# Kernel tuning notes

Measured on AMD Instinct MI355X. Metric: run time of the kernel, lower is better.

The kernel has to match this reference:

```python
import jax, jax.numpy as jnp
import numpy as np

N_NODES = 100000
N_EDGES = 6_400_000
IN_DIM = 128


def gcn_conv(x, W, b, row, col, ew):
    """PyG GCNConv(normalize=True, add_self_loops=True) forward."""
    n = x.shape[0]
    loop = jnp.arange(n)
    row_sl = jnp.concatenate([row, loop])
    col_sl = jnp.concatenate([col, loop])
    ew_sl = jnp.concatenate([ew, jnp.ones((n,), ew.dtype)])
    # symmetric normalization: deg^{-1/2}[src] * w * deg^{-1/2}[dst]
    deg = jax.ops.segment_sum(ew_sl, col_sl, num_segments=n)
    safe_deg = jnp.where(deg > 0, deg, 1.0)
    dis = jnp.where(deg > 0, jax.lax.rsqrt(safe_deg), 0.0)
    norm = dis[row_sl] * ew_sl * dis[col_sl]
    h = x @ W  # [n, out_dim] linear transform first (small out_dim)
    # gather source features, scale, scatter-add into targets
    out = jax.ops.segment_sum(norm[:, None] * h[row_sl], col_sl, num_segments=n)
    return out + b


def setup_inputs() -> dict:
    key = jax.random.key(0)
    ks = jax.random.split(key, 12)
    X = jax.random.normal(ks[0], (N_NODES, IN_DIM), dtype=jnp.float32)
    edge_index = jax.random.randint(ks[1], (2, N_EDGES), 0, N_NODES, dtype=jnp.int64)
    edge_weight = jax.random.uniform(ks[2], (N_EDGES,), dtype=jnp.float32)

    def glorot(k, fan_in, fan_out):
        lim = np.sqrt(6.0 / (fan_in + fan_out)).astype(np.float32)
        return jax.random.uniform(k, (fan_in, fan_out), minval=-lim, maxval=lim, dtype=jnp.float32)

    return {
        "X": X,
        "edge_index": edge_index,
        "edge_weight": edge_weight,
        "W1": glorot(ks[3], IN_DIM, 12), "b1": jnp.zeros((12,), jnp.float32),
        "W2": glorot(ks[4], 12, 6), "b2": jnp.zeros((6,), jnp.float32),
        "W3": glorot(ks[5], 6, 3), "b3": jnp.zeros((3,), jnp.float32),
        "Wl": glorot(ks[6], 3, 1), "bl": jnp.zeros((1,), jnp.float32),
    }


def reference(X, edge_index, edge_weight, W1, b1, W2, b2, W3, b3, Wl, bl):
    row, col = edge_index[0], edge_index[1]
    h = jax.nn.relu(gcn_conv(X, W1, b1, row, col, edge_weight))
    # dropout p=0.2 is identity in eval mode
    h = jax.nn.relu(gcn_conv(h, W2, b2, row, col, edge_weight))
    h = jax.nn.relu(gcn_conv(h, W3, b3, row, col, edge_weight))
    out = jax.nn.sigmoid(h @ Wl + bl)
    return out.squeeze(1)  # [N]
```

## Files before the change

### kernel.cpp

```cpp
#include <hip/hip_runtime.h>
#include <cstdint>
#include <cstddef>

#define RANGE    128
#define RSHIFT   7
#define MAXBUCK  800
#define CSHIFT   12
#define CRANGE   4096
#define MAXC     32
#define FPB      32
#define CH_CNT   8192
#define CH_SC    4096
#define EPT      16
#define PAD      16
#define WSTR     132

typedef _Float16 h8 __attribute__((ext_vector_type(8)));

__global__ void zero_pad_kernel(int* __restrict__ p, int n) {
    int i = blockIdx.x * blockDim.x + threadIdx.x;
    if (i < n) p[i * PAD] = 0;
}

__global__ void count_kernel(const int* __restrict__ col, int* __restrict__ fcnt,
                             int nfine, int E) {
    __shared__ int lcnt[MAXBUCK];
    int tid = threadIdx.x;
    for (int i = tid; i < nfine; i += blockDim.x) lcnt[i] = 0;
    __syncthreads();
    int base = blockIdx.x * CH_CNT;
    int end  = min(E, base + CH_CNT);
    for (int e = base + tid; e < end; e += blockDim.x)
        atomicAdd(&lcnt[col[e] >> RSHIFT], 1);
    __syncthreads();
    for (int i = tid; i < nfine; i += blockDim.x)
        if (lcnt[i]) atomicAdd(&fcnt[i * PAD], lcnt[i]);
}

__global__ void scan_kernel(const int* __restrict__ fcnt, int* __restrict__ fbase,
                            int* __restrict__ fcur, int* __restrict__ cbase,
                            int* __restrict__ ccur, int* __restrict__ row_ptr,
                            int nfine, int ncoarse, int N, int E) {
    __shared__ int lds[1024];
    int T = threadIdx.x;
    int s = (T < nfine) ? fcnt[T * PAD] : 0;
    lds[T] = s;
    __syncthreads();
    for (int off = 1; off < 1024; off <<= 1) {
        int v = (T >= off) ? lds[T - off] : 0;
        __syncthreads();
        lds[T] += v;
        __syncthreads();
    }
    int excl = lds[T] - s;
    if (T < nfine) { fbase[T] = excl; fcur[T * PAD] = excl; }
    if ((T & (FPB - 1)) == 0 && (T >> 5) < ncoarse) {
        cbase[T >> 5] = excl;
        ccur[(T >> 5) * PAD] = excl;
    }
    if (T == 0) { fbase[nfine] = E; cbase[ncoarse] = E; row_ptr[N] = E; }
}

__global__ void coarse_scatter_kernel(const int* __restrict__ row, const int* __restrict__ col,
                                      const float* __restrict__ ew, int* __restrict__ ccur,
                                      uint2* __restrict__ partA, int ncoarse, int E) {
    __shared__ uint2 stage[CH_SC];
    __shared__ unsigned char sb[CH_SC];
    __shared__ int lcnt[MAXC], lofs[MAXC], gofs[MAXC];
    __shared__ int total_s;
    int tid = threadIdx.x;
    if (tid < MAXC) lcnt[tid] = 0;
    __syncthreads();
    int base = blockIdx.x * CH_SC;
    int cnt  = min(E - base, CH_SC);

    uint2 rec[EPT]; int rnk[EPT]; int bb[EPT];
#pragma unroll
    for (int k = 0; k < EPT; k++) {
        int idx = tid + (k << 8);
        if (idx < cnt) {
            int e = base + idx;
            int c = col[e];
            int b = c >> CSHIFT;
            bb[k]  = b;
            rec[k] = make_uint2((unsigned)row[e] | ((unsigned)(c & (CRANGE - 1)) << 17),
                                __float_as_uint(ew[e]));
            rnk[k] = atomicAdd(&lcnt[b], 1);
        }
    }
    __syncthreads();
    if (tid == 0) {
        int run = 0;
        for (int i = 0; i < ncoarse; i++) { lofs[i] = run; run += lcnt[i]; }
        total_s = run;
    }
    __syncthreads();
    if (tid < ncoarse) {
        int c = lcnt[tid];
        if (c) {
            int g = atomicAdd(&ccur[tid * PAD], c);
            gofs[tid] = g - lofs[tid];
        }
    }
#pragma unroll
    for (int k = 0; k < EPT; k++) {
        int idx = tid + (k << 8);
        if (idx < cnt) {
            int p = lofs[bb[k]] + rnk[k];
            stage[p] = rec[k];
            sb[p] = (unsigned char)bb[k];
        }
    }
    __syncthreads();
    int total = total_s;
    for (int i = tid; i < total; i += 256)
        partA[gofs[sb[i]] + i] = stage[i];
}

__global__ void fine_scatter_kernel(const uint2* __restrict__ partA, const int* __restrict__ cbase,
                                    int* __restrict__ fcur, uint2* __restrict__ partB,
                                    int nfine, int ncoarse, int E) {
    __shared__ uint2 stage[CH_SC];
    __shared__ unsigned short sb[CH_SC];
    __shared__ int lcnt[MAXBUCK], lofs[MAXBUCK], gofs[MAXBUCK];
    __shared__ int tmp[256];
    __shared__ int scb[MAXC + 1];
    __shared__ int rlo_s, total_s;
    int tid = threadIdx.x;
    int base = blockIdx.x * CH_SC;
    int cnt  = min(E - base, CH_SC);
    if (tid <= ncoarse) scb[tid] = cbase[tid];
    for (int i = tid; i < nfine; i += 256) lcnt[i] = 0;
    if (tid == 0) {
        int r = 0;
        while (r < ncoarse - 1 && cbase[r + 1] <= base) ++r;
        rlo_s = r;
    }
    __syncthreads();
    int rlo = rlo_s;

    uint2 rec[EPT]; int rnk[EPT]; int ff[EPT];
#pragma unroll
    for (int k = 0; k < EPT; k++) {
        int idx = tid + (k << 8);
        if (idx < cnt) {
            int e = base + idx;
            uint2 v = partA[e];
            int r = rlo;
            while (e >= scb[r + 1]) ++r;
            int col12 = (int)((v.x >> 17) & (CRANGE - 1));
            int f = (r << 5) | (col12 >> RSHIFT);
            ff[k]  = f;
            rec[k] = make_uint2((v.x & 0x1FFFFu) | ((unsigned)(col12 & (RANGE - 1)) << 17), v.y);
            rnk[k] = atomicAdd(&lcnt[f], 1);
        }
    }
    __syncthreads();
    {
        const int Cc = (nfine + 255) >> 8;
        int b0 = tid * Cc;
        int s = 0;
        for (int i = 0; i < Cc; i++) {
            int idx = b0 + i;
            if (idx < nfine) s += lcnt[idx];
        }
        tmp[tid] = s;
        __syncthreads();
        for (int off = 1; off < 256; off <<= 1) {
            int v = (tid >= off) ? tmp[tid - off] : 0;
            __syncthreads();
            tmp[tid] += v;
            __syncthreads();
        }
        int run = tmp[tid] - s;
        for (int i = 0; i < Cc; i++) {
            int idx = b0 + i;
            if (idx < nfine) { lofs[idx] = run; run += lcnt[idx]; }
        }
        if (tid == 255) total_s = tmp[255];
    }
    __syncthreads();
    for (int i = tid; i < nfine; i += 256) {
        int c = lcnt[i];
        if (c) {
            int g = atomicAdd(&fcur[i * PAD], c);
            gofs[i] = g - lofs[i];
        }
    }
#pragma unroll
    for (int k = 0; k < EPT; k++) {
        int idx = tid + (k << 8);
        if (idx < cnt) {
            int p = lofs[ff[k]] + rnk[k];
            stage[p] = rec[k];
            sb[p] = (unsigned short)ff[k];
        }
    }
    __syncthreads();
    int total = total_s;
    for (int i = tid; i < total; i += 256)
        partB[gofs[sb[i]] + i] = stage[i];
}

__global__ void bucket_csr_kernel(const uint2* __restrict__ part, const int* __restrict__ bbase,
                                  int* __restrict__ row_ptr, float* __restrict__ dis,
                                  uint2* __restrict__ csr, int N) {
    __shared__ int   scnt[RANGE];
    __shared__ int   sscan[RANGE];
    __shared__ float sdeg[RANGE];
    __shared__ float sdis[RANGE];
    int b = blockIdx.x, tid = threadIdx.x;
    int s = bbase[b], t = bbase[b + 1];
    if (tid < RANGE) { scnt[tid] = 0; sdeg[tid] = 1.0f; }
    __syncthreads();
    for (int e = s + tid; e < t; e += blockDim.x) {
        uint2 r = part[e];
        int c = (r.x >> 17) & (RANGE - 1);
        atomicAdd(&scnt[c], 1);
        atomicAdd(&sdeg[c], __uint_as_float(r.y));
    }
    __syncthreads();
    int cnt_t = 0;
    if (tid < RANGE) { cnt_t = scnt[tid]; sscan[tid] = cnt_t; }
    __syncthreads();
    for (int off = 1; off < RANGE; off <<= 1) {
        int v = 0;
        if (tid < RANGE && tid >= off) v = sscan[tid - off];
        __syncthreads();
        if (tid < RANGE) sscan[tid] += v;
        __syncthreads();
    }
    if (tid < RANGE) {
        int excl = sscan[tid] - cnt_t;
        int node = b * RANGE + tid;
        float dn = rsqrtf(sdeg[tid]);
        sdis[tid] = dn;
        if (node < N) {
            row_ptr[node] = s + excl;
            dis[node] = dn;
        }
        scnt[tid] = excl;
    }
    __syncthreads();
    for (int e = s + tid; e < t; e += blockDim.x) {
        uint2 r = part[e];
        int c   = (r.x >> 17) & (RANGE - 1);
        int src = (int)(r.x & 0x1FFFFu);
        float v = sdis[c] * __uint_as_float(r.y);
        int off = atomicAdd(&scnt[c], 1);
        csr[s + off] = make_uint2((unsigned)src, __float_as_uint(v));
    }
}

__global__ void lin1_kernel(const float* __restrict__ X, const float* __restrict__ W1,
                            const float* __restrict__ dis, uint4* __restrict__ t1, int n) {
    __shared__ float w1t[12 * WSTR];
    int tid = threadIdx.x;
    for (int i = tid; i < 128 * 12; i += 256) {
        int k = i / 12, o = i - k * 12;
        w1t[o * WSTR + k] = W1[i];
    }
    __syncthreads();
    int gt   = blockIdx.x * 256 + tid;
    int node = gt >> 3;
    int sub  = gt & 7;
    if (node >= n) return;

    const float4* xp = (const float4*)(X + (size_t)node * 128 + sub * 16);
    float4 x0 = xp[0], x1 = xp[1], x2 = xp[2], x3 = xp[3];

    float res[12];
#pragma unroll
    for (int o = 0; o < 12; o++) {
        const float4* wp = (const float4*)(w1t + o * WSTR + sub * 16);
        float4 w0 = wp[0], w1v = wp[1], w2 = wp[2], w3 = wp[3];
        float s;
        s  = x0.x * w0.x + x0.y * w0.y + x0.z * w0.z + x0.w * w0.w;
        s += x1.x * w1v.x + x1.y * w1v.y + x1.z * w1v.z + x1.w * w1v.w;
        s += x2.x * w2.x + x2.y * w2.y + x2.z * w2.z + x2.w * w2.w;
        s += x3.x * w3.x + x3.y * w3.y + x3.z * w3.z + x3.w * w3.w;
        res[o] = s;
    }
#pragma unroll
    for (int o = 0; o < 12; o++) {
        res[o] += __shfl_xor(res[o], 1, 64);
        res[o] += __shfl_xor(res[o], 2, 64);
        res[o] += __shfl_xor(res[o], 4, 64);
    }
    if (sub == 0) {
        h8 a, b;
#pragma unroll
        for (int o = 0; o < 8; o++) a[o] = (_Float16)res[o];
#pragma unroll
        for (int o = 0; o < 4; o++) b[o] = (_Float16)res[8 + o];
#pragma unroll
        for (int o = 4; o < 8; o++) b[o] = (_Float16)0.f;
        uint4 ua = __builtin_bit_cast(uint4, a);
        uint4 ub = __builtin_bit_cast(uint4, b);
        ub.z = __float_as_uint(dis[node]);
        ub.w = 0u;
        uint4* dst = t1 + (size_t)node * 2;
        dst[0] = ua;
        dst[1] = ub;
    }
}

template <int DIN, int ROWW, int DOUT, bool LAST>
__global__ void agg_kernel(const int* __restrict__ row_ptr, const uint2* __restrict__ csr,
                           const uint4* __restrict__ hin,
                           const float* __restrict__ b_this, const float* __restrict__ W_next,
                           const float* __restrict__ b_next, void* __restrict__ hout_v, int n) {
    int gt   = blockIdx.x * blockDim.x + threadIdx.x;
    int node = gt >> 3;
    int sub  = gt & 7;
    if (node >= n) return;
    int start = row_ptr[node];
    int end   = row_ptr[node + 1];
    float acc[DIN];
#pragma unroll
    for (int d = 0; d < DIN; d++) acc[d] = 0.f;

    for (int e = start + sub; e < end; e += 8) {
        unsigned long long raw =
            __builtin_nontemporal_load((const unsigned long long*)(csr + e));
        int src    = (int)(unsigned)raw;
        float ewdd = __uint_as_float((unsigned)(raw >> 32));
        const uint4* hr = hin + (size_t)src * ROWW;
        if constexpr (DIN == 12) {
            uint4 ua = hr[0], ub = hr[1];
            float norm = ewdd * __uint_as_float(ub.z);
            h8 a = __builtin_bit_cast(h8, ua);
            h8 b = __builtin_bit_cast(h8, ub);
#pragma unroll
            for (int d = 0; d < 8; d++) acc[d] += norm * (float)a[d];
#pragma unroll
            for (int d = 0; d < 4; d++) acc[8 + d] += norm * (float)b[d];
        } else if constexpr (DIN == 6) {
            uint4 u = hr[0];
            float norm = ewdd * __uint_as_float(u.w);
            h8 a = __builtin_bit_cast(h8, u);
#pragma unroll
            for (int d = 0; d < 6; d++) acc[d] += norm * (float)a[d];
        } else {
            uint4 u = hr[0];
            float norm = ewdd * __uint_as_float(u.z);
            h8 a = __builtin_bit_cast(h8, u);
#pragma unroll
            for (int d = 0; d < 3; d++) acc[d] += norm * (float)a[d];
        }
    }

#pragma unroll
    for (int d = 0; d < DIN; d++) {
        acc[d] += __shfl_xor(acc[d], 1, 64);
        acc[d] += __shfl_xor(acc[d], 2, 64);
        acc[d] += __shfl_xor(acc[d], 4, 64);
    }

    if (sub == 0) {
        const uint4* hn = hin + (size_t)node * ROWW;
        float v[DIN];
        float dn;
        if constexpr (DIN == 12) {
            uint4 ua = hn[0], ub = hn[1];
            dn = __uint_as_float(ub.z);
            float s2 = dn * dn;
            h8 a = __builtin_bit_cast(h8, ua);
            h8 b = __builtin_bit_cast(h8, ub);
#pragma unroll
            for (int d = 0; d < 8; d++) v[d] = fmaxf(acc[d] + s2 * (float)a[d] + b_this[d], 0.f);
#pragma unroll
            for (int d = 0; d < 4; d++) v[8 + d] = fmaxf(acc[8 + d] + s2 * (float)b[d] + b_this[8 + d], 0.f);
        } else if constexpr (DIN == 6) {
            uint4 u = hn[0];
            dn = __uint_as_float(u.w);
            float s2 = dn * dn;
            h8 a = __builtin_bit_cast(h8, u);
#pragma unroll
            for (int d = 0; d < 6; d++) v[d] = fmaxf(acc[d] + s2 * (float)a[d] + b_this[d], 0.f);
        } else {
            uint4 u = hn[0];
            dn = __uint_as_float(u.z);
            float s2 = dn * dn;
            h8 a = __builtin_bit_cast(h8, u);
#pragma unroll
            for (int d = 0; d < 3; d++) v[d] = fmaxf(acc[d] + s2 * (float)a[d] + b_this[d], 0.f);
        }
        if constexpr (!LAST) {
            float o[DOUT];
#pragma unroll
            for (int oo = 0; oo < DOUT; oo++) {
                float z = 0.f;
#pragma unroll
                for (int d = 0; d < DIN; d++) z += v[d] * W_next[d * DOUT + oo];
                o[oo] = z;
            }
            h8 w;
#pragma unroll
            for (int oo = 0; oo < 8; oo++) w[oo] = (_Float16)0.f;
#pragma unroll
            for (int oo = 0; oo < DOUT; oo++) w[oo] = (_Float16)o[oo];
            uint4 uw = __builtin_bit_cast(uint4, w);
            if constexpr (DOUT == 6) uw.w = __float_as_uint(dn);
            else                     uw.z = __float_as_uint(dn);
            ((uint4*)hout_v)[node] = uw;
        } else {
            float z = b_next[0];
#pragma unroll
            for (int d = 0; d < DIN; d++) z += v[d] * W_next[d];
            ((float*)hout_v)[node] = 1.0f / (1.0f + expf(-z));
        }
    }
}

extern "C" void kernel_launch(void* const* d_in, const int* in_sizes, int n_in,
                              void* d_out, int out_size, void* d_ws, size_t ws_size,
                              hipStream_t stream) {
    const float* X  = (const float*)d_in[0];
    const int*   ei = (const int*)d_in[1];
    const float* ew = (const float*)d_in[2];
    const float* W1 = (const float*)d_in[3];
    const float* b1 = (const float*)d_in[4];
    const float* W2 = (const float*)d_in[5];
    const float* b2 = (const float*)d_in[6];
    const float* W3 = (const float*)d_in[7];
    const float* b3 = (const float*)d_in[8];
    const float* Wl = (const float*)d_in[9];
    const float* bl = (const float*)d_in[10];
    float* out = (float*)d_out;

    const int N = in_sizes[0] / 128;
    const int E = in_sizes[1] / 2;
    const int* row = ei;
    const int* col = ei + E;
    const int nfine   = (N + RANGE - 1) >> RSHIFT;
    const int ncoarse = (N + CRANGE - 1) >> CSHIFT;

    char* ws = (char*)d_ws;
    size_t off = 0;
    auto carve = [&](size_t bytes) -> void* {
        void* p = ws + off;
        off += (bytes + 255) & ~(size_t)255;
        return p;
    };
    int*   fcnt    = (int*)  carve((size_t)MAXBUCK * PAD * 4);
    int*   fcur    = (int*)  carve((size_t)MAXBUCK * PAD * 4);
    int*   ccur    = (int*)  carve((size_t)MAXC * PAD * 4);
    int*   cbase   = (int*)  carve((size_t)(MAXC + 1) * 4);
    int*   fbase   = (int*)  carve((size_t)(MAXBUCK + 1) * 4);
    int*   row_ptr = (int*)  carve((size_t)(N + 1) * 4);
    float* dis     = (float*)carve((size_t)N * 4);
    uint2* partA   = (uint2*)carve((size_t)E * 8);
    uint2* partB   = (uint2*)carve((size_t)E * 8);
    uint2* csr = partA;
    uint4* t1  = (uint4*)partB;
    uint4* t2  = t1 + (size_t)N * 2;
    uint4* t3  = t2 + (size_t)N;
    (void)ws_size; (void)n_in; (void)out_size;

    const int bCnt = (E + CH_CNT - 1) / CH_CNT;
    const int bSc  = (E + CH_SC - 1) / CH_SC;
    const int bL   = ((size_t)N * 8 + 255) / 256;
    const int bA   = ((size_t)N * 8 + 255) / 256;

    zero_pad_kernel<<<(nfine + 255) / 256, 256, 0, stream>>>(fcnt, nfine);
    count_kernel<<<bCnt, 256, 0, stream>>>(col, fcnt, nfine, E);
    scan_kernel<<<1, 1024, 0, stream>>>(fcnt, fbase, fcur, cbase, ccur, row_ptr,
                                        nfine, ncoarse, N, E);
    coarse_scatter_kernel<<<bSc, 256, 0, stream>>>(row, col, ew, ccur, partA, ncoarse, E);
    fine_scatter_kernel<<<bSc, 256, 0, stream>>>(partA, cbase, fcur, partB, nfine, ncoarse, E);
    bucket_csr_kernel<<<nfine, 256, 0, stream>>>(partB, fbase, row_ptr, dis, csr, N);
    lin1_kernel<<<bL, 256, 0, stream>>>(X, W1, dis, t1, N);
    agg_kernel<12, 2, 6, false><<<bA, 256, 0, stream>>>(row_ptr, csr, t1, b1, W2, nullptr, t2, N);
    agg_kernel< 6, 1, 3, false><<<bA, 256, 0, stream>>>(row_ptr, csr, t2, b2, W3, nullptr, t3, N);
    agg_kernel< 3, 1, 1, true ><<<bA, 256, 0, stream>>>(row_ptr, csr, t3, b3, Wl, bl, out, N);
}
```

Baseline: 557.2 us.

## Split per-bucket CSR build into chunked histogram, scan, and staged write kernels

Replaces the single bucket_csr_kernel, which used one block per 128-node bucket, with three kernels. A chunk-parallel node histogram uses shared-memory atomics and global merges. A per-bucket scan then computes row_ptr and dis. A chunk-parallel CSR write stages records in shared memory and writes them out coalesced, with each block locating the buckets it covers by binary search over fbase. The aim is better load balance and coalescing for the roughly 800 uneven buckets, paid for with two extra passes over partB, more launches and global atomics per node.

```diff
diff --git a/kernel.cpp b/kernel.cpp
--- a/kernel.cpp
+++ b/kernel.cpp
@@ -14,12 +14,18 @@
 #define EPT      16
 #define PAD      16
 #define WSTR     132
+#define SPAN     4
 
 typedef _Float16 h8 __attribute__((ext_vector_type(8)));
 
 __global__ void zero_pad_kernel(int* __restrict__ p, int n) {
     int i = blockIdx.x * blockDim.x + threadIdx.x;
     if (i < n) p[i * PAD] = 0;
+}
+
+__global__ void init_nodes_kernel(int* __restrict__ ncnt, float* __restrict__ ndeg, int N) {
+    int i = blockIdx.x * blockDim.x + threadIdx.x;
+    if (i < N) { ncnt[i] = 0; ndeg[i] = 1.0f; }
 }
 
 __global__ void count_kernel(const int* __restrict__ col, int* __restrict__ fcnt,
@@ -202,54 +208,155 @@
         partB[gofs[sb[i]] + i] = stage[i];
 }
 
-__global__ void bucket_csr_kernel(const uint2* __restrict__ part, const int* __restrict__ bbase,
-                                  int* __restrict__ row_ptr, float* __restrict__ dis,
-                                  uint2* __restrict__ csr, int N) {
-    __shared__ int   scnt[RANGE];
-    __shared__ int   sscan[RANGE];
-    __shared__ float sdeg[RANGE];
-    __shared__ float sdis[RANGE];
+__global__ void node_hist_kernel(const uint2* __restrict__ partB, const int* __restrict__ fbase,
+                                 int* __restrict__ ncnt, float* __restrict__ ndeg,
+                                 int nfine, int E) {
+    __shared__ int   lcnt[SPAN * RANGE];
+    __shared__ float ldeg[SPAN * RANGE];
+    __shared__ int sfb[SPAN + 1];
+    __shared__ int blo_s;
+    int tid = threadIdx.x;
+    int base = blockIdx.x * CH_SC;
+    int cnt  = min(E - base, CH_SC);
+    if (tid == 0) {
+        int lo = 0, hi = nfine;
+        while (lo + 1 < hi) { int mid = (lo + hi) >> 1; if (fbase[mid] <= base) lo = mid; else hi = mid; }
+        blo_s = lo;
+    }
+    for (int i = tid; i < SPAN * RANGE; i += 256) { lcnt[i] = 0; ldeg[i] = 0.f; }
+    __syncthreads();
+    int blo = blo_s;
+    if (tid <= SPAN) sfb[tid] = fbase[min(blo + tid, nfine)];
+    __syncthreads();
+#pragma unroll
+    for (int k = 0; k < EPT; k++) {
+        int idx = tid + (k << 8);
+        if (idx < cnt) {
+            int e = base + idx;
+            uint2 v = partB[e];
+            int b = 0;
+            while (e >= sfb[b + 1]) ++b;
+            int slot = (b << RSHIFT) | (int)((v.x >> 17) & (RANGE - 1));
+            atomicAdd(&lcnt[slot], 1);
+            atomicAdd(&ldeg[slot], __uint_as_float(v.y));
+        }
+    }
+    __syncthreads();
+    for (int i = tid; i < SPAN * RANGE; i += 256) {
+        if (lcnt[i]) {
+            int node = (blo + (i >> RSHIFT)) * RANGE + (i & (RANGE - 1));
+            atomicAdd(&ncnt[node], lcnt[i]);
+            atomicAdd(&ndeg[node], ldeg[i]);
+        }
+    }
+}
+
+__global__ void row_ptr_dis_kernel(const int* __restrict__ fbase, const int* __restrict__ ncnt,
+                                   const float* __restrict__ ndeg, int* __restrict__ row_ptr,
+                                   int* __restrict__ ncur, float* __restrict__ dis, int N) {
+    __shared__ int sscan[RANGE];
     int b = blockIdx.x, tid = threadIdx.x;
-    int s = bbase[b], t = bbase[b + 1];
-    if (tid < RANGE) { scnt[tid] = 0; sdeg[tid] = 1.0f; }
-    __syncthreads();
-    for (int e = s + tid; e < t; e += blockDim.x) {
-        uint2 r = part[e];
-        int c = (r.x >> 17) & (RANGE - 1);
-        atomicAdd(&scnt[c], 1);
-        atomicAdd(&sdeg[c], __uint_as_float(r.y));
-    }
-    __syncthreads();
-    int cnt_t = 0;
-    if (tid < RANGE) { cnt_t = scnt[tid]; sscan[tid] = cnt_t; }
+    int node = b * RANGE + tid;
+    int c = (node < N) ? ncnt[node] : 0;
+    sscan[tid] = c;
     __syncthreads();
     for (int off = 1; off < RANGE; off <<= 1) {
-        int v = 0;
-        if (tid < RANGE && tid >= off) v = sscan[tid - off];
+        int v = (tid >= off) ? sscan[tid - off] : 0;
         __syncthreads();
-        if (tid < RANGE) sscan[tid] += v;
+        sscan[tid] += v;
         __syncthreads();
     }
-    if (tid < RANGE) {
-        int excl = sscan[tid] - cnt_t;
-        int node = b * RANGE + tid;
-        float dn = rsqrtf(sdeg[tid]);
-        sdis[tid] = dn;
-        if (node < N) {
-            row_ptr[node] = s + excl;
-            dis[node] = dn;
-        }
-        scnt[tid] = excl;
-    }
-    __syncthreads();
-    for (int e = s + tid; e < t; e += blockDim.x) {
-        uint2 r = part[e];
-        int c   = (r.x >> 17) & (RANGE - 1);
-        int src = (int)(r.x & 0x1FFFFu);
-        float v = sdis[c] * __uint_as_float(r.y);
-        int off = atomicAdd(&scnt[c], 1);
-        csr[s + off] = make_uint2((unsigned)src, __float_as_uint(v));
-    }
+    if (node < N) {
+        int rp = fbase[b] + sscan[tid] - c;
+        row_ptr[node] = rp;
+        ncur[node]    = rp;
+        dis[node]     = rsqrtf(ndeg[node]);
+    }
+}
+
+__global__ void csr_write_kernel(const uint2* __restrict__ partB, const int* __restrict__ fbase,
+                                 const float* __restrict__ dis, int* __restrict__ ncur,
+                                 uint2* __restrict__ csr, int nfine, int E, int N) {
+    __shared__ uint2 stage[CH_SC];
+    __shared__ unsigned short sb[CH_SC];
+    __shared__ int   lcnt[SPAN * RANGE], lofs[SPAN * RANGE], gofs[SPAN * RANGE];
+    __shared__ float sdis[SPAN * RANGE];
+    __shared__ int tmp[256];
+    __shared__ int sfb[SPAN + 1];
+    __shared__ int blo_s, total_s;
+    int tid = threadIdx.x;
+    int base = blockIdx.x * CH_SC;
+    int cnt  = min(E - base, CH_SC);
+    if (tid == 0) {
+        int lo = 0, hi = nfine;
+        while (lo + 1 < hi) { int mid = (lo + hi) >> 1; if (fbase[mid] <= base) lo = mid; else hi = mid; }
+        blo_s = lo;
+    }
+    for (int i = tid; i < SPAN * RANGE; i += 256) lcnt[i] = 0;
+    __syncthreads();
+    int blo = blo_s;
+    if (tid <= SPAN) sfb[tid] = fbase[min(blo + tid, nfine)];
+    for (int i = tid; i < SPAN * RANGE; i += 256) {
+        int node = (blo + (i >> RSHIFT)) * RANGE + (i & (RANGE - 1));
+        sdis[i] = (node < N) ? dis[node] : 0.f;
+    }
+    __syncthreads();
+
+    uint2 rec[EPT]; int rnk[EPT]; int ss[EPT];
+#pragma unroll
+    for (int k = 0; k < EPT; k++) {
+        int idx = tid + (k << 8);
+        if (idx < cnt) {
+            int e = base + idx;
+            uint2 v = partB[e];
+            int b = 0;
+            while (e >= sfb[b + 1]) ++b;
+            int slot = (b << RSHIFT) | (int)((v.x >> 17) & (RANGE - 1));
+            ss[k]  = slot;
+            rec[k] = make_uint2(v.x & 0x1FFFFu,
+                                __float_as_uint(sdis[slot] * __uint_as_float(v.y)));
+            rnk[k] = atomicAdd(&lcnt[slot], 1);
+        }
+    }
+    __syncthreads();
+    {
+        int b0 = tid * 2;
+        int s = lcnt[b0] + lcnt[b0 + 1];
+        tmp[tid] = s;
+        __syncthreads();
+        for (int off = 1; off < 256; off <<= 1) {
+            int v = (tid >= off) ? tmp[tid - off] : 0;
+            __syncthreads();
+            tmp[tid] += v;
+            __syncthreads();
+        }
+        int run = tmp[tid] - s;
+        lofs[b0] = run;
+        lofs[b0 + 1] = run + lcnt[b0];
+        if (tid == 255) total_s = tmp[255];
+    }
+    __syncthreads();
+    for (int i = tid; i < SPAN * RANGE; i += 256) {
+        int c = lcnt[i];
+        if (c) {
+            int node = (blo + (i >> RSHIFT)) * RANGE + (i & (RANGE - 1));
+            int g = atomicAdd(&ncur[node], c);
+            gofs[i] = g - lofs[i];
+        }
+    }
+#pragma unroll
+    for (int k = 0; k < EPT; k++) {
+        int idx = tid + (k << 8);
+        if (idx < cnt) {
+            int p = lofs[ss[k]] + rnk[k];
+            stage[p] = rec[k];
+            sb[p] = (unsigned short)ss[k];
+        }
+    }
+    __syncthreads();
+    int total = total_s;
+    for (int i = tid; i < total; i += 256)
+        csr[gofs[sb[i]] + i] = stage[i];
 }
 
 __global__ void lin1_kernel(const float* __restrict__ X, const float* __restrict__ W1,
@@ -450,6 +557,9 @@
     int*   fbase   = (int*)  carve((size_t)(MAXBUCK + 1) * 4);
     int*   row_ptr = (int*)  carve((size_t)(N + 1) * 4);
     float* dis     = (float*)carve((size_t)N * 4);
+    int*   ncnt    = (int*)  carve((size_t)N * 4);
+    float* ndeg    = (float*)carve((size_t)N * 4);
+    int*   ncur    = (int*)  carve((size_t)N * 4);
     uint2* partA   = (uint2*)carve((size_t)E * 8);
     uint2* partB   = (uint2*)carve((size_t)E * 8);
     uint2* csr = partA;
@@ -462,14 +572,18 @@
     const int bSc  = (E + CH_SC - 1) / CH_SC;
     const int bL   = ((size_t)N * 8 + 255) / 256;
     const int bA   = ((size_t)N * 8 + 255) / 256;
+    const int bN   = (N + 255) / 256;
 
     zero_pad_kernel<<<(nfine + 255) / 256, 256, 0, stream>>>(fcnt, nfine);
+    init_nodes_kernel<<<bN, 256, 0, stream>>>(ncnt, ndeg, N);
     count_kernel<<<bCnt, 256, 0, stream>>>(col, fcnt, nfine, E);
     scan_kernel<<<1, 1024, 0, stream>>>(fcnt, fbase, fcur, cbase, ccur, row_ptr,
                                         nfine, ncoarse, N, E);
     coarse_scatter_kernel<<<bSc, 256, 0, stream>>>(row, col, ew, ccur, partA, ncoarse, E);
     fine_scatter_kernel<<<bSc, 256, 0, stream>>>(partA, cbase, fcur, partB, nfine, ncoarse, E);
-    bucket_csr_kernel<<<nfine, 256, 0, stream>>>(partB, fbase, row_ptr, dis, csr, N);
+    node_hist_kernel<<<bSc, 256, 0, stream>>>(partB, fbase, ncnt, ndeg, nfine, E);
+    row_ptr_dis_kernel<<<nfine, RANGE, 0, stream>>>(fbase, ncnt, ndeg, row_ptr, ncur, dis, N);
+    csr_write_kernel<<<bSc, 256, 0, stream>>>(partB, fbase, dis, ncur, csr, nfine, E, N);
     lin1_kernel<<<bL, 256, 0, stream>>>(X, W1, dis, t1, N);
     agg_kernel<12, 2, 6, false><<<bA, 256, 0, stream>>>(row_ptr, csr, t1, b1, W2, nullptr, t2, N);
     agg_kernel< 6, 1, 3, false><<<bA, 256, 0, stream>>>(row_ptr, csr, t2, b2, W3, nullptr, t3, N);
```

After: 567.6 us. No clear change (+1.9%).
